# Kernel tuning notes

Measured on AMD Instinct MI355X. Metric: run time of the kernel, lower is better.

Reference implementation:

```python
import jax, jax.numpy as jnp
import numpy as np

N = 20000      # nodes
E = 320000     # edges (avg degree 16)
F_IN = 14
F_OUT = 9
H = 128        # hidden
L = 6          # message passing layers
ED = 3         # edge_dim
MSG_IN = 2 * H + ED  # 259


def _w(k, shape):
    return jax.random.normal(k, shape, jnp.float32) / np.sqrt(shape[0]).astype(np.float32)


def setup_inputs() -> dict:
    key = jax.random.key(0)
    ks = jax.random.split(key, 16)
    x = jax.random.normal(ks[0], (N, F_IN), jnp.float32)
    edge_index = jax.random.randint(ks[1], (2, E), 0, N, jnp.int64)
    edge_attr = jax.random.normal(ks[2], (E, ED), jnp.float32)
    # encoder: Linear(14,128) -> SiLU -> Linear(128,128)
    enc_w1 = _w(ks[3], (F_IN, H)); enc_b1 = jnp.zeros((H,), jnp.float32)
    enc_w2 = _w(ks[4], (H, H));    enc_b2 = jnp.zeros((H,), jnp.float32)
    # L EdgeConv layers: MLP(259->128) -> SiLU -> (128->128), stacked on leading dim
    kc = jax.random.split(ks[5], 2 * L)
    conv_w1 = jnp.stack([_w(kc[i], (MSG_IN, H)) for i in range(L)])
    conv_b1 = jnp.zeros((L, H), jnp.float32)
    conv_w2 = jnp.stack([_w(kc[L + i], (H, H)) for i in range(L)])
    conv_b2 = jnp.zeros((L, H), jnp.float32)
    # decoder: 128->128 SiLU 128->64 SiLU 64->9
    dec_w1 = _w(ks[6], (H, H));       dec_b1 = jnp.zeros((H,), jnp.float32)
    dec_w2 = _w(ks[7], (H, H // 2));  dec_b2 = jnp.zeros((H // 2,), jnp.float32)
    dec_w3 = _w(ks[8], (H // 2, F_OUT)); dec_b3 = jnp.zeros((F_OUT,), jnp.float32)
    return dict(x=x, edge_index=edge_index, edge_attr=edge_attr,
                enc_w1=enc_w1, enc_b1=enc_b1, enc_w2=enc_w2, enc_b2=enc_b2,
                conv_w1=conv_w1, conv_b1=conv_b1, conv_w2=conv_w2, conv_b2=conv_b2,
                dec_w1=dec_w1, dec_b1=dec_b1, dec_w2=dec_w2, dec_b2=dec_b2,
                dec_w3=dec_w3, dec_b3=dec_b3)


def _mlp2(x, w1, b1, w2, b2):
    return jnp.dot(jax.nn.silu(jnp.dot(x, w1) + b1), w2) + b2


def reference(x, edge_index, edge_attr,
              enc_w1, enc_b1, enc_w2, enc_b2,
              conv_w1, conv_b1, conv_w2, conv_b2,
              dec_w1, dec_b1, dec_w2, dec_b2, dec_w3, dec_b3):
    src, dst = edge_index[0], edge_index[1]
    # in-degree for mean aggregation (computed once; structure is fixed)
    deg = jnp.maximum(
        jax.ops.segment_sum(jnp.ones((E,), jnp.float32), dst, num_segments=N), 1.0)
    h = _mlp2(x, enc_w1, enc_b1, enc_w2, enc_b2)  # (N, H)
    for l in range(L):
        # gather-compute-scatter EdgeConv: msg MLP on [h_dst, h_src, edge_attr]
        m_in = jnp.concatenate([h[dst], h[src], edge_attr], axis=-1)  # (E, 2H+ED)
        m = _mlp2(m_in, conv_w1[l], conv_b1[l], conv_w2[l], conv_b2[l])  # (E, H)
        agg = jax.ops.segment_sum(m, dst, num_segments=N) / deg[:, None]  # (N, H)
        h = h + agg  # residual; dropout is identity in eval mode
    h = jax.nn.silu(jnp.dot(h, dec_w1) + dec_b1)
    h = jax.nn.silu(jnp.dot(h, dec_w2) + dec_b2)
    return jnp.dot(h, dec_w3) + dec_b3  # (N, F_OUT)
```

## Files before the change

### kernel.cpp

```cpp
#include <hip/hip_runtime.h>
#include <hip/hip_bf16.h>

#define NN 20000
#define EE 320000
#define HD 128

typedef _Float16 half8 __attribute__((ext_vector_type(8)));
typedef _Float16 half4 __attribute__((ext_vector_type(4)));
typedef _Float16 half2v __attribute__((ext_vector_type(2)));
typedef float floatx4 __attribute__((ext_vector_type(4)));
typedef float float2v __attribute__((ext_vector_type(2)));

__device__ __forceinline__ float silu_f(float x){
  float e = __expf(-x);
  return x * __builtin_amdgcn_rcpf(1.f + e);
}

__device__ __forceinline__ bool ei_is64(const int* __restrict__ ei){
  return (ei[1] | ei[3] | ei[5] | ei[7]) == 0;
}
__device__ __forceinline__ int ei_src(const int* __restrict__ ei, int e, bool is64){
  return is64 ? ei[2*(size_t)e] : ei[e];
}
__device__ __forceinline__ int ei_dst(const int* __restrict__ ei, int e, bool is64){
  return is64 ? ei[2*(size_t)EE + 2*(size_t)e] : ei[EE + e];
}

__global__ __launch_bounds__(256) void sentinel_kernel(float* __restrict__ out, int n, float val){
  int i = blockIdx.x*256 + threadIdx.x;
  if (i < n) out[i] = val;
}

__global__ __launch_bounds__(256) void pack_all_kernel(const float* __restrict__ cw1,
                                                       const float* __restrict__ cw2,
                                                       const float* __restrict__ dw1,
                                                       const float* __restrict__ dw2,
                                                       _Float16* __restrict__ w1p,
                                                       _Float16* __restrict__ w2p,
                                                       _Float16* __restrict__ w1dp,
                                                       _Float16* __restrict__ w2dp,
                                                       int* __restrict__ cur){
  int idx = blockIdx.x*256 + threadIdx.x;
  if (idx >= 319488){
    int j = idx - 319488;
    if (j < NN) cur[j] = 0;
    return;
  }
  if (idx < 196608){
    int j   = idx & 7;
    int ln  = (idx >> 3) & 63;
    int rest= idx >> 9;
    int cb  = rest & 15;
    int rest2 = rest >> 4;
    int ks  = rest2 & 3;
    int l   = rest2 >> 2;
    int k = ks*32 + (ln>>4)*8 + j;
    int c = cb*16 + (ln&15);
    float v = (c < 128) ? cw1[(size_t)l*33152 + (size_t)k*128 + c]
                        : cw1[(size_t)l*33152 + (size_t)(128+k)*128 + (c-128)];
    w1p[idx] = (_Float16)v;
  } else if (idx < 294912){
    int t = idx - 196608;
    int j   = t & 7;
    int ln  = (t >> 3) & 63;
    int rest= t >> 9;
    int cb  = rest & 7;
    int rest2 = rest >> 3;
    int ks  = rest2 & 3;
    int l   = rest2 >> 2;
    int k = ks*32 + (ln>>4)*8 + j;
    int c = cb*16 + (ln&15);
    w2p[t] = (_Float16)cw2[(size_t)l*16384 + (size_t)k*128 + c];
  } else {
    int t2 = idx - 294912;
    if (t2 < 16384){
      int j = t2 & 7, ln = (t2>>3)&63, cb = (t2>>9)&7, ks = t2>>12;
      int k = ks*32 + (ln>>4)*8 + j;
      int c = cb*16 + (ln&15);
      w1dp[t2] = (_Float16)dw1[(size_t)k*128 + c];
    } else {
      int t = t2 - 16384;
      int j = t & 7, ln = (t>>3)&63, cb = (t>>9)&3, ks = t>>11;
      int k = ks*32 + (ln>>4)*8 + j;
      int c = cb*16 + (ln&15);
      w2dp[t] = (_Float16)dw2[(size_t)k*64 + c];
    }
  }
}

__global__ __launch_bounds__(256) void count_kernel(const int* __restrict__ ei,
                                                    int* __restrict__ cnt,
                                                    int* __restrict__ rank){
  int e = blockIdx.x*256 + threadIdx.x;
  bool is64 = ei_is64(ei);
  rank[e] = atomicAdd(&cnt[ei_dst(ei, e, is64)], 1);
}

__global__ __launch_bounds__(1024) void scan_kernel(const int* __restrict__ cntcur,
                                                    int* __restrict__ row_start,
                                                    float* __restrict__ invd){
  __shared__ int part[1024];
  const int t = threadIdx.x;
  const int base = t*20;
  int loc[20];
  int sum = 0;
  #pragma unroll
  for (int i=0;i<20;++i){
    int n = base+i;
    int v = (n < NN) ? cntcur[n] : 0;
    loc[i] = sum; sum += v;
  }
  part[t] = sum;
  __syncthreads();
  for (int off=1; off<1024; off<<=1){
    int v = (t >= off) ? part[t-off] : 0;
    __syncthreads();
    part[t] += v;
    __syncthreads();
  }
  int pre = (t > 0) ? part[t-1] : 0;
  #pragma unroll
  for (int i=0;i<20;++i){
    int n = base+i;
    if (n < NN){
      int rs = pre + loc[i];
      int deg = ((i<19)?loc[i+1]:sum) - loc[i];
      row_start[n] = rs;
      invd[n] = (deg > 0) ? 1.f/(float)deg : 0.f;
    }
  }
  if (t == 1023) row_start[NN] = part[1023];
}

__global__ __launch_bounds__(128) void scatter_encoder_kernel(
    const int* __restrict__ ei, const float* __restrict__ eattr,
    const int* __restrict__ rstart, const int* __restrict__ rank,
    int4* __restrict__ rec,
    const float* __restrict__ x, const float* __restrict__ w1, const float* __restrict__ b1,
    const float* __restrict__ w2, const float* __restrict__ b2,
    float* __restrict__ h, _Float16* __restrict__ hh)
{
  __shared__ float xs[16][14];
  __shared__ float s1[16][128];
  const int tid = threadIdx.x;

  if (blockIdx.x < 2500){
    int e = blockIdx.x*128 + tid;
    bool is64 = ei_is64(ei);
    int s = ei_src(ei, e, is64);
    int d = ei_dst(ei, e, is64);
    int pos = rstart[d] + rank[e];
    int4 r;
    r.x = __float_as_int(eattr[(size_t)e*3+0]);
    r.y = __float_as_int(eattr[(size_t)e*3+1]);
    r.z = __float_as_int(eattr[(size_t)e*3+2]);
    r.w = s*256;
    rec[pos] = r;
    return;
  }

  const int n0 = (blockIdx.x - 2500)*16;
  for (int idx=tid; idx<224; idx+=128){
    int i = idx/14, k = idx%14;
    xs[i][k] = x[(size_t)(n0+i)*14 + k];
  }
  __syncthreads();
  const int o = tid;
  float acc[16];
  float bv = b1[o];
  #pragma unroll
  for (int i=0;i<16;++i) acc[i] = bv;
  for (int k=0;k<14;++k){
    float w = w1[k*128+o];
    #pragma unroll
    for (int i=0;i<16;++i) acc[i] += xs[i][k]*w;
  }
  #pragma unroll
  for (int i=0;i<16;++i) s1[i][o] = silu_f(acc[i]);
  __syncthreads();
  float bv2 = b2[o];
  #pragma unroll
  for (int i=0;i<16;++i) acc[i] = bv2;
  for (int k=0;k<128;k+=4){
    float w0=w2[(k+0)*128+o], w1v=w2[(k+1)*128+o], w2v=w2[(k+2)*128+o], w3v=w2[(k+3)*128+o];
    #pragma unroll
    for (int i=0;i<16;++i){
      float4 sv = *(const float4*)&s1[i][k];
      acc[i] += sv.x*w0 + sv.y*w1v + sv.z*w2v + sv.w*w3v;
    }
  }
  #pragma unroll
  for (int i=0;i<16;++i){
    size_t off = (size_t)(n0+i)*HD + o;
    h[off] = acc[i];
    hh[off] = (_Float16)acc[i];
  }
}

__global__ __launch_bounds__(256) void proj_kernel(
    const _Float16* __restrict__ hh, const _Float16* __restrict__ w1p,
    const float* __restrict__ b1, _Float16* __restrict__ UV)
{
  const int tid = threadIdx.x;
  const int wv  = tid >> 6;
  const int ln  = tid & 63;
  const int q   = ln >> 4;
  const int m   = ln & 15;
  const int n0  = blockIdx.x*16;

  floatx4 acc[4];
  #pragma unroll
  for (int j=0;j<4;++j) acc[j] = (floatx4){0.f,0.f,0.f,0.f};

  #pragma unroll
  for (int ks=0; ks<4; ++ks){
    half8 a = *(const half8*)(hh + (size_t)(n0+m)*HD + ks*32 + q*8);
    const _Float16* wb = w1p + (size_t)(ks*16*64 + ln)*8;
    #pragma unroll
    for (int j=0; j<4; ++j){
      half8 b = *(const half8*)(wb + (size_t)(wv*4+j)*512);
      acc[j] = __builtin_amdgcn_mfma_f32_16x16x32_f16(a, b, acc[j], 0,0,0);
    }
  }
  #pragma unroll
  for (int j=0; j<4; ++j){
    const int c = (wv*4+j)*16 + m;
    const float bias = (c < 128) ? b1[c] : 0.f;
    #pragma unroll
    for (int r=0;r<4;++r)
      UV[(size_t)(n0+q*4+r)*256 + c] = (_Float16)(acc[j][r] + bias);
  }
}

__device__ __forceinline__ float2v edge_contrib(int4 r, half2v v, float2v u,
                                                float2v wc0, float2v wc1, float2v wc2){
  float2v p = u;
  p += __int_as_float(r.x) * wc0;
  p += __int_as_float(r.y) * wc1;
  p += __int_as_float(r.z) * wc2;
  p[0] += (float)v[0];
  p[1] += (float)v[1];
  float2v s;
  s[0] = silu_f(p[0]);
  s[1] = silu_f(p[1]);
  return s;
}

__global__ __launch_bounds__(256) void edge_agg_kernel(
    const _Float16* __restrict__ UV, const int* __restrict__ row_start,
    const int4* __restrict__ rec,
    const float* __restrict__ w1e, const float* __restrict__ invd,
    _Float16* __restrict__ S)
{
  const int tid = threadIdx.x;
  const int wv  = __builtin_amdgcn_readfirstlane(tid >> 6);
  const int ln  = tid & 63;
  const int n   = blockIdx.x*4 + wv;
  const int c0  = ln*2;

  const float2v wc0 = *(const float2v*)(w1e +   0 + c0);
  const float2v wc1 = *(const float2v*)(w1e + 128 + c0);
  const float2v wc2 = *(const float2v*)(w1e + 256 + c0);

  half2v uvp = *(const half2v*)(UV + (size_t)n*256 + c0);
  float2v u; u[0] = (float)uvp[0]; u[1] = (float)uvp[1];

  const int rs = row_start[n], re = row_start[n+1];
  float2v a0 = {0.f,0.f}, a1 = {0.f,0.f}, a2 = {0.f,0.f}, a3 = {0.f,0.f};

  const int nq = (re - rs) >> 2;
  int e = rs;
  for (int q = 0; q < nq; ++q, e += 4){
    const int4 r0 = rec[e+0];
    const int4 r1 = rec[e+1];
    const int4 r2 = rec[e+2];
    const int4 r3 = rec[e+3];
    const half2v v0 = *(const half2v*)(UV + (size_t)r0.w + 128 + c0);
    const half2v v1 = *(const half2v*)(UV + (size_t)r1.w + 128 + c0);
    const half2v v2 = *(const half2v*)(UV + (size_t)r2.w + 128 + c0);
    const half2v v3 = *(const half2v*)(UV + (size_t)r3.w + 128 + c0);
    a0 += edge_contrib(r0, v0, u, wc0, wc1, wc2);
    a1 += edge_contrib(r1, v1, u, wc0, wc1, wc2);
    a2 += edge_contrib(r2, v2, u, wc0, wc1, wc2);
    a3 += edge_contrib(r3, v3, u, wc0, wc1, wc2);
  }
  if (e < re){
    const int e1 = (e+1 < re) ? e+1 : e;
    const int e2 = (e+2 < re) ? e+2 : e;
    const int4 r0 = rec[e];
    const int4 r1 = rec[e1];
    const int4 r2 = rec[e2];
    const half2v v0 = *(const half2v*)(UV + (size_t)r0.w + 128 + c0);
    const half2v v1 = *(const half2v*)(UV + (size_t)r1.w + 128 + c0);
    const half2v v2 = *(const half2v*)(UV + (size_t)r2.w + 128 + c0);
    a0 += edge_contrib(r0, v0, u, wc0, wc1, wc2);
    if (e+1 < re) a1 += edge_contrib(r1, v1, u, wc0, wc1, wc2);
    if (e+2 < re) a2 += edge_contrib(r2, v2, u, wc0, wc1, wc2);
  }
  float2v a = (a0 + a1) + (a2 + a3);
  const float iv = invd[n];
  half2v outv; outv[0] = (_Float16)(a[0]*iv); outv[1] = (_Float16)(a[1]*iv);
  *(half2v*)(S + (size_t)n*HD + c0) = outv;
}

__global__ __launch_bounds__(256) void node_proj_kernel(
    const _Float16* __restrict__ S, const _Float16* __restrict__ w2p,
    const float* __restrict__ b2, const float* __restrict__ invd,
    float* __restrict__ h,
    const _Float16* __restrict__ w1pn, const float* __restrict__ b1n,
    _Float16* __restrict__ UV, int do_proj,
    const _Float16* __restrict__ w1dp, const float* __restrict__ db1,
    const _Float16* __restrict__ w2dp, const float* __restrict__ db2,
    const float* __restrict__ dw3, const float* __restrict__ db3,
    float* __restrict__ out, int do_dec)
{
  __shared__ _Float16 hl[16][136];
  __shared__ __align__(16) char ubuf[8576];
  float    (*dl)[132]  = (float(*)[132])ubuf;
  _Float16 (*d1)[136]  = (_Float16(*)[136])ubuf;
  float    (*s2m)[66]  = (float(*)[66])(ubuf + 4352);

  const int tid = threadIdx.x;
  const int wv  = tid >> 6;
  const int ln  = tid & 63;
  const int q   = ln >> 4;
  const int m   = ln & 15;
  const int n0  = blockIdx.x*16;

  floatx4 acc[2];
  acc[0] = (floatx4){0.f,0.f,0.f,0.f};
  acc[1] = (floatx4){0.f,0.f,0.f,0.f};
  #pragma unroll
  for (int ks=0; ks<4; ++ks){
    half8 a = *(const half8*)(S + (size_t)(n0+m)*HD + ks*32 + q*8);
    const _Float16* wb = w2p + (size_t)(ks*8*64 + ln)*8;
    #pragma unroll
    for (int j=0;j<2;++j){
      half8 b = *(const half8*)(wb + (size_t)(wv*2+j)*512);
      acc[j] = __builtin_amdgcn_mfma_f32_16x16x32_f16(a, b, acc[j], 0,0,0);
    }
  }
  #pragma unroll
  for (int j=0; j<2; ++j){
    const int c = (wv*2+j)*16 + m;
    #pragma unroll
    for (int r=0;r<4;++r) dl[q*4+r][c] = acc[j][r];
  }
  __syncthreads();

  {
    const int idx = tid*8;
    const int row = idx >> 7;
    const int col = idx & 127;
    const float g = (invd[n0 + row] > 0.f) ? 1.f : 0.f;
    float4 h0 = *(const float4*)&h[(size_t)(n0+row)*HD + col];
    float4 h1 = *(const float4*)&h[(size_t)(n0+row)*HD + col + 4];
    float4 b0 = *(const float4*)&b2[col];
    float4 b1v = *(const float4*)&b2[col + 4];
    float4 d0 = *(const float4*)&dl[row][col];
    float4 d1v = *(const float4*)&dl[row][col + 4];
    h0.x += d0.x + g*b0.x;  h0.y += d0.y + g*b0.y;
    h0.z += d0.z + g*b0.z;  h0.w += d0.w + g*b0.w;
    h1.x += d1v.x + g*b1v.x; h1.y += d1v.y + g*b1v.y;
    h1.z += d1v.z + g*b1v.z; h1.w += d1v.w + g*b1v.w;
    if (!do_dec){
      *(float4*)&h[(size_t)(n0+row)*HD + col]     = h0;
      *(float4*)&h[(size_t)(n0+row)*HD + col + 4] = h1;
    }
    half4 p0, p1;
    p0[0]=(_Float16)h0.x; p0[1]=(_Float16)h0.y; p0[2]=(_Float16)h0.z; p0[3]=(_Float16)h0.w;
    p1[0]=(_Float16)h1.x; p1[1]=(_Float16)h1.y; p1[2]=(_Float16)h1.z; p1[3]=(_Float16)h1.w;
    *(half4*)&hl[row][col]     = p0;
    *(half4*)&hl[row][col + 4] = p1;
  }
  __syncthreads();

  if (do_proj){
    floatx4 acc2[4];
    #pragma unroll
    for (int j=0;j<4;++j) acc2[j] = (floatx4){0.f,0.f,0.f,0.f};
    #pragma unroll
    for (int ks=0; ks<4; ++ks){
      half8 a = *(const half8*)&hl[m][ks*32 + q*8];
      const _Float16* wb = w1pn + (size_t)(ks*16*64 + ln)*8;
      #pragma unroll
      for (int j=0; j<4; ++j){
        half8 b = *(const half8*)(wb + (size_t)(wv*4+j)*512);
        acc2[j] = __builtin_amdgcn_mfma_f32_16x16x32_f16(a, b, acc2[j], 0,0,0);
      }
    }
    #pragma unroll
    for (int j=0; j<4; ++j){
      const int c = (wv*4+j)*16 + m;
      const float bias = (c < 128) ? b1n[c] : 0.f;
      #pragma unroll
      for (int r=0;r<4;++r)
        UV[(size_t)(n0+q*4+r)*256 + c] = (_Float16)(acc2[j][r] + bias);
    }
  }

  if (do_dec){
    floatx4 acc1[2];
    acc1[0] = (floatx4){0.f,0.f,0.f,0.f};
    acc1[1] = (floatx4){0.f,0.f,0.f,0.f};
    #pragma unroll
    for (int ks=0; ks<4; ++ks){
      half8 a = *(const half8*)&hl[m][ks*32 + q*8];
      const _Float16* wb = w1dp + (size_t)(ks*8*64 + ln)*8;
      #pragma unroll
      for (int j=0; j<2; ++j){
        half8 b = *(const half8*)(wb + (size_t)(wv*2+j)*512);
        acc1[j] = __builtin_amdgcn_mfma_f32_16x16x32_f16(a, b, acc1[j], 0,0,0);
      }
    }
    __syncthreads();
    #pragma unroll
    for (int j=0; j<2; ++j){
      const int c = (wv*2+j)*16 + m;
      const float bv = db1[c];
      #pragma unroll
      for (int r=0;r<4;++r)
        d1[q*4+r][c] = (_Float16)silu_f(acc1[j][r] + bv);
    }
    __syncthreads();

    floatx4 acc2 = (floatx4){0.f,0.f,0.f,0.f};
    #pragma unroll
    for (int ks=0; ks<4; ++ks){
      half8 a = *(const half8*)&d1[m][ks*32 + q*8];
      const _Float16* wb = w2dp + (size_t)(ks*4*64 + ln)*8;
      half8 b = *(const half8*)(wb + (size_t)wv*512);
      acc2 = __builtin_amdgcn_mfma_f32_16x16x32_f16(a, b, acc2, 0,0,0);
    }
    {
      const int c = wv*16 + m;
      const float bv = db2[c];
      #pragma unroll
      for (int r=0;r<4;++r)
        s2m[q*4+r][c] = silu_f(acc2[r] + bv);
    }
    __syncthreads();

    if (tid < 144){
      int i = tid/9, oo = tid%9;
      float a = db3[oo];
      #pragma unroll 8
      for (int k=0;k<64;++k) a += s2m[i][k]*dw3[k*9+oo];
      out[(size_t)(n0+i)*9 + oo] = a;
    }
  }
}

constexpr size_t OFF_H    = 0;
constexpr size_t OFF_HH   = 10240000;
constexpr size_t OFF_UV   = 15360000;
constexpr size_t OFF_S    = 25600000;
constexpr size_t OFF_INVD = 30720000;
constexpr size_t OFF_RS   = 30800000;
constexpr size_t OFF_CUR  = 30880064;
constexpr size_t OFF_REC  = 30960064;
constexpr size_t OFF_RANK = 36080064;
constexpr size_t OFF_W1P  = 37360064;
constexpr size_t OFF_W2P  = 37753280;
constexpr size_t OFF_DW1P = 37949888;
constexpr size_t OFF_DW2P = 37982656;
constexpr size_t WS_NEEDED= 37999040;

extern "C" void kernel_launch(void* const* d_in, const int* in_sizes, int n_in,
                              void* d_out, int out_size, void* d_ws, size_t ws_size,
                              hipStream_t stream)
{
  float* out = (float*)d_out;
  const int nout_blk = (out_size + 255)/256;

  static const int EXP_SIZES[17] = {280000,640000,960000,1792,128,16384,128,
                                    198912,768,98304,768,16384,128,8192,64,576,9};
  if (n_in != 17){
    sentinel_kernel<<<nout_blk, 256, 0, stream>>>(out, out_size, 2.0e7f + (float)n_in*1.0e3f);
    return;
  }
  for (int i = 0; i < 17; ++i){
    if (in_sizes[i] != EXP_SIZES[i]){
      int sz = in_sizes[i] < 99999 ? in_sizes[i] : 99999;
      sentinel_kernel<<<nout_blk, 256, 0, stream>>>(out, out_size,
          1.0e7f + (float)i*1.0e5f + (float)sz);
      return;
    }
  }
  if (ws_size < WS_NEEDED){
    sentinel_kernel<<<nout_blk, 256, 0, stream>>>(out, out_size, 1.0e6f);
    return;
  }

  const float* x       = (const float*)d_in[0];
  const int*   ei      = (const int*)  d_in[1];
  const float* eattr   = (const float*)d_in[2];
  const float* enc_w1  = (const float*)d_in[3];
  const float* enc_b1  = (const float*)d_in[4];
  const float* enc_w2  = (const float*)d_in[5];
  const float* enc_b2  = (const float*)d_in[6];
  const float* conv_w1 = (const float*)d_in[7];
  const float* conv_b1 = (const float*)d_in[8];
  const float* conv_w2 = (const float*)d_in[9];
  const float* conv_b2 = (const float*)d_in[10];
  const float* dec_w1  = (const float*)d_in[11];
  const float* dec_b1  = (const float*)d_in[12];
  const float* dec_w2  = (const float*)d_in[13];
  const float* dec_b2  = (const float*)d_in[14];
  const float* dec_w3  = (const float*)d_in[15];
  const float* dec_b3  = (const float*)d_in[16];

  char* ws = (char*)d_ws;
  float*    h     = (float*)   (ws + OFF_H);
  _Float16* hh    = (_Float16*)(ws + OFF_HH);
  _Float16* UV    = (_Float16*)(ws + OFF_UV);
  _Float16* S     = (_Float16*)(ws + OFF_S);
  float*    invd  = (float*)   (ws + OFF_INVD);
  int*      rstart= (int*)     (ws + OFF_RS);
  int*      cur   = (int*)     (ws + OFF_CUR);
  int4*     rec   = (int4*)    (ws + OFF_REC);
  int*      rank  = (int*)     (ws + OFF_RANK);
  _Float16* w1p   = (_Float16*)(ws + OFF_W1P);
  _Float16* w2p   = (_Float16*)(ws + OFF_W2P);
  _Float16* w1dp  = (_Float16*)(ws + OFF_DW1P);
  _Float16* w2dp  = (_Float16*)(ws + OFF_DW2P);

  pack_all_kernel<<<1327, 256, 0, stream>>>(conv_w1, conv_w2, dec_w1, dec_w2,
                                            w1p, w2p, w1dp, w2dp, cur);
  count_kernel<<<EE/256, 256, 0, stream>>>(ei, cur, rank);
  scan_kernel<<<1, 1024, 0, stream>>>(cur, rstart, invd);
  scatter_encoder_kernel<<<3750, 128, 0, stream>>>(ei, eattr, rstart, rank, rec,
                                                   x, enc_w1, enc_b1, enc_w2, enc_b2,
                                                   h, hh);
  proj_kernel<<<NN/16, 256, 0, stream>>>(hh, w1p, conv_b1, UV);
  for (int l=0; l<6; ++l){
    edge_agg_kernel<<<NN/4, 256, 0, stream>>>(UV, rstart, rec,
                                              conv_w1 + (size_t)l*33152 + 32768,
                                              invd, S);
    const int lp = (l < 5) ? l+1 : 0;
    node_proj_kernel<<<NN/16, 256, 0, stream>>>(S, w2p + (size_t)l*16384,
                                                conv_b2 + (size_t)l*128, invd, h,
                                                w1p + (size_t)lp*32768,
                                                conv_b1 + (size_t)lp*128,
                                                UV, (l < 5) ? 1 : 0,
                                                w1dp, dec_b1, w2dp, dec_b2,
                                                dec_w3, dec_b3, out,
                                                (l == 5) ? 1 : 0);
  }
}
```

Baseline: 372.4 us.

## Fuse edge aggregation and node projection into one per-layer kernel

Merges the edge gather/aggregate kernel and the node update/projection kernel into a single 1024-thread kernel per layer. Each block handles 16 nodes, one wave per node, and keeps the aggregated messages in shared memory instead of writing and re-reading a global S buffer. The UV buffer is double-buffered (ping-pong) so the next layer's projections can be written while neighbours still read the current one. This removes one launch per layer and the S round trip, at the cost of larger blocks, idle waves in the smaller GEMM stages, and an extra global buffer.

```diff
diff --git a/kernel.cpp b/kernel.cpp
--- a/kernel.cpp
+++ b/kernel.cpp
@@ -246,74 +246,20 @@
   return s;
 }
 
-__global__ __launch_bounds__(256) void edge_agg_kernel(
-    const _Float16* __restrict__ UV, const int* __restrict__ row_start,
-    const int4* __restrict__ rec,
+__global__ __launch_bounds__(1024, 8) void layer_kernel(
+    const _Float16* __restrict__ UVc, _Float16* __restrict__ UVn,
+    const int* __restrict__ row_start, const int4* __restrict__ rec,
     const float* __restrict__ w1e, const float* __restrict__ invd,
-    _Float16* __restrict__ S)
-{
-  const int tid = threadIdx.x;
-  const int wv  = __builtin_amdgcn_readfirstlane(tid >> 6);
-  const int ln  = tid & 63;
-  const int n   = blockIdx.x*4 + wv;
-  const int c0  = ln*2;
-
-  const float2v wc0 = *(const float2v*)(w1e +   0 + c0);
-  const float2v wc1 = *(const float2v*)(w1e + 128 + c0);
-  const float2v wc2 = *(const float2v*)(w1e + 256 + c0);
-
-  half2v uvp = *(const half2v*)(UV + (size_t)n*256 + c0);
-  float2v u; u[0] = (float)uvp[0]; u[1] = (float)uvp[1];
-
-  const int rs = row_start[n], re = row_start[n+1];
-  float2v a0 = {0.f,0.f}, a1 = {0.f,0.f}, a2 = {0.f,0.f}, a3 = {0.f,0.f};
-
-  const int nq = (re - rs) >> 2;
-  int e = rs;
-  for (int q = 0; q < nq; ++q, e += 4){
-    const int4 r0 = rec[e+0];
-    const int4 r1 = rec[e+1];
-    const int4 r2 = rec[e+2];
-    const int4 r3 = rec[e+3];
-    const half2v v0 = *(const half2v*)(UV + (size_t)r0.w + 128 + c0);
-    const half2v v1 = *(const half2v*)(UV + (size_t)r1.w + 128 + c0);
-    const half2v v2 = *(const half2v*)(UV + (size_t)r2.w + 128 + c0);
-    const half2v v3 = *(const half2v*)(UV + (size_t)r3.w + 128 + c0);
-    a0 += edge_contrib(r0, v0, u, wc0, wc1, wc2);
-    a1 += edge_contrib(r1, v1, u, wc0, wc1, wc2);
-    a2 += edge_contrib(r2, v2, u, wc0, wc1, wc2);
-    a3 += edge_contrib(r3, v3, u, wc0, wc1, wc2);
-  }
-  if (e < re){
-    const int e1 = (e+1 < re) ? e+1 : e;
-    const int e2 = (e+2 < re) ? e+2 : e;
-    const int4 r0 = rec[e];
-    const int4 r1 = rec[e1];
-    const int4 r2 = rec[e2];
-    const half2v v0 = *(const half2v*)(UV + (size_t)r0.w + 128 + c0);
-    const half2v v1 = *(const half2v*)(UV + (size_t)r1.w + 128 + c0);
-    const half2v v2 = *(const half2v*)(UV + (size_t)r2.w + 128 + c0);
-    a0 += edge_contrib(r0, v0, u, wc0, wc1, wc2);
-    if (e+1 < re) a1 += edge_contrib(r1, v1, u, wc0, wc1, wc2);
-    if (e+2 < re) a2 += edge_contrib(r2, v2, u, wc0, wc1, wc2);
-  }
-  float2v a = (a0 + a1) + (a2 + a3);
-  const float iv = invd[n];
-  half2v outv; outv[0] = (_Float16)(a[0]*iv); outv[1] = (_Float16)(a[1]*iv);
-  *(half2v*)(S + (size_t)n*HD + c0) = outv;
-}
-
-__global__ __launch_bounds__(256) void node_proj_kernel(
-    const _Float16* __restrict__ S, const _Float16* __restrict__ w2p,
-    const float* __restrict__ b2, const float* __restrict__ invd,
+    const _Float16* __restrict__ w2p, const float* __restrict__ b2,
     float* __restrict__ h,
     const _Float16* __restrict__ w1pn, const float* __restrict__ b1n,
-    _Float16* __restrict__ UV, int do_proj,
+    int do_proj,
     const _Float16* __restrict__ w1dp, const float* __restrict__ db1,
     const _Float16* __restrict__ w2dp, const float* __restrict__ db2,
     const float* __restrict__ dw3, const float* __restrict__ db3,
     float* __restrict__ out, int do_dec)
 {
+  __shared__ _Float16 Sl[16][136];
   __shared__ _Float16 hl[16][136];
   __shared__ __align__(16) char ubuf[8576];
   float    (*dl)[132]  = (float(*)[132])ubuf;
@@ -321,123 +267,136 @@
   float    (*s2m)[66]  = (float(*)[66])(ubuf + 4352);
 
   const int tid = threadIdx.x;
-  const int wv  = tid >> 6;
+  const int w   = __builtin_amdgcn_readfirstlane(tid >> 6);
   const int ln  = tid & 63;
   const int q   = ln >> 4;
   const int m   = ln & 15;
   const int n0  = blockIdx.x*16;
 
-  floatx4 acc[2];
-  acc[0] = (floatx4){0.f,0.f,0.f,0.f};
-  acc[1] = (floatx4){0.f,0.f,0.f,0.f};
-  #pragma unroll
-  for (int ks=0; ks<4; ++ks){
-    half8 a = *(const half8*)(S + (size_t)(n0+m)*HD + ks*32 + q*8);
-    const _Float16* wb = w2p + (size_t)(ks*8*64 + ln)*8;
-    #pragma unroll
-    for (int j=0;j<2;++j){
-      half8 b = *(const half8*)(wb + (size_t)(wv*2+j)*512);
-      acc[j] = __builtin_amdgcn_mfma_f32_16x16x32_f16(a, b, acc[j], 0,0,0);
-    }
-  }
-  #pragma unroll
-  for (int j=0; j<2; ++j){
-    const int c = (wv*2+j)*16 + m;
-    #pragma unroll
-    for (int r=0;r<4;++r) dl[q*4+r][c] = acc[j][r];
+  {
+    const int n  = n0 + w;
+    const int c0 = ln*2;
+    const float2v wc0 = *(const float2v*)(w1e +   0 + c0);
+    const float2v wc1 = *(const float2v*)(w1e + 128 + c0);
+    const float2v wc2 = *(const float2v*)(w1e + 256 + c0);
+
+    half2v uvp = *(const half2v*)(UVc + (size_t)n*256 + c0);
+    float2v u; u[0] = (float)uvp[0]; u[1] = (float)uvp[1];
+
+    const int rs = row_start[n], re = row_start[n+1];
+    float2v a0 = {0.f,0.f}, a1 = {0.f,0.f}, a2 = {0.f,0.f}, a3 = {0.f,0.f};
+
+    const int nq = (re - rs) >> 2;
+    int e = rs;
+    for (int qq = 0; qq < nq; ++qq, e += 4){
+      const int4 r0 = rec[e+0];
+      const int4 r1 = rec[e+1];
+      const int4 r2 = rec[e+2];
+      const int4 r3 = rec[e+3];
+      const half2v v0 = *(const half2v*)(UVc + (size_t)r0.w + 128 + c0);
+      const half2v v1 = *(const half2v*)(UVc + (size_t)r1.w + 128 + c0);
+      const half2v v2 = *(const half2v*)(UVc + (size_t)r2.w + 128 + c0);
+      const half2v v3 = *(const half2v*)(UVc + (size_t)r3.w + 128 + c0);
+      a0 += edge_contrib(r0, v0, u, wc0, wc1, wc2);
+      a1 += edge_contrib(r1, v1, u, wc0, wc1, wc2);
+      a2 += edge_contrib(r2, v2, u, wc0, wc1, wc2);
+      a3 += edge_contrib(r3, v3, u, wc0, wc1, wc2);
+    }
+    if (e < re){
+      const int e1 = (e+1 < re) ? e+1 : e;
+      const int e2 = (e+2 < re) ? e+2 : e;
+      const int4 r0 = rec[e];
+      const int4 r1 = rec[e1];
+      const int4 r2 = rec[e2];
+      const half2v v0 = *(const half2v*)(UVc + (size_t)r0.w + 128 + c0);
+      const half2v v1 = *(const half2v*)(UVc + (size_t)r1.w + 128 + c0);
+      const half2v v2 = *(const half2v*)(UVc + (size_t)r2.w + 128 + c0);
+      a0 += edge_contrib(r0, v0, u, wc0, wc1, wc2);
+      if (e+1 < re) a1 += edge_contrib(r1, v1, u, wc0, wc1, wc2);
+      if (e+2 < re) a2 += edge_contrib(r2, v2, u, wc0, wc1, wc2);
+    }
+    float2v a = (a0 + a1) + (a2 + a3);
+    const float iv = invd[n];
+    half2v outv; outv[0] = (_Float16)(a[0]*iv); outv[1] = (_Float16)(a[1]*iv);
+    *(half2v*)&Sl[w][c0] = outv;
   }
   __syncthreads();
 
+  if (w < 8){
+    floatx4 acc = (floatx4){0.f,0.f,0.f,0.f};
+    #pragma unroll
+    for (int ks=0; ks<4; ++ks){
+      half8 a = *(const half8*)&Sl[m][ks*32 + q*8];
+      half8 b = *(const half8*)(w2p + (size_t)(ks*8*64 + ln)*8 + (size_t)w*512);
+      acc = __builtin_amdgcn_mfma_f32_16x16x32_f16(a, b, acc, 0,0,0);
+    }
+    const int c = w*16 + m;
+    #pragma unroll
+    for (int r=0;r<4;++r) dl[q*4+r][c] = acc[r];
+  }
+  __syncthreads();
+
   {
-    const int idx = tid*8;
-    const int row = idx >> 7;
-    const int col = idx & 127;
+    const int row = w;
+    const int col = ln*2;
     const float g = (invd[n0 + row] > 0.f) ? 1.f : 0.f;
-    float4 h0 = *(const float4*)&h[(size_t)(n0+row)*HD + col];
-    float4 h1 = *(const float4*)&h[(size_t)(n0+row)*HD + col + 4];
-    float4 b0 = *(const float4*)&b2[col];
-    float4 b1v = *(const float4*)&b2[col + 4];
-    float4 d0 = *(const float4*)&dl[row][col];
-    float4 d1v = *(const float4*)&dl[row][col + 4];
-    h0.x += d0.x + g*b0.x;  h0.y += d0.y + g*b0.y;
-    h0.z += d0.z + g*b0.z;  h0.w += d0.w + g*b0.w;
-    h1.x += d1v.x + g*b1v.x; h1.y += d1v.y + g*b1v.y;
-    h1.z += d1v.z + g*b1v.z; h1.w += d1v.w + g*b1v.w;
-    if (!do_dec){
-      *(float4*)&h[(size_t)(n0+row)*HD + col]     = h0;
-      *(float4*)&h[(size_t)(n0+row)*HD + col + 4] = h1;
-    }
-    half4 p0, p1;
-    p0[0]=(_Float16)h0.x; p0[1]=(_Float16)h0.y; p0[2]=(_Float16)h0.z; p0[3]=(_Float16)h0.w;
-    p1[0]=(_Float16)h1.x; p1[1]=(_Float16)h1.y; p1[2]=(_Float16)h1.z; p1[3]=(_Float16)h1.w;
-    *(half4*)&hl[row][col]     = p0;
-    *(half4*)&hl[row][col + 4] = p1;
+    float2 hv = *(const float2*)&h[(size_t)(n0+row)*HD + col];
+    float2 bv = *(const float2*)&b2[col];
+    float2 dv = *(const float2*)&dl[row][col];
+    hv.x += dv.x + g*bv.x;
+    hv.y += dv.y + g*bv.y;
+    if (!do_dec)
+      *(float2*)&h[(size_t)(n0+row)*HD + col] = hv;
+    half2v p; p[0] = (_Float16)hv.x; p[1] = (_Float16)hv.y;
+    *(half2v*)&hl[row][col] = p;
   }
   __syncthreads();
 
   if (do_proj){
-    floatx4 acc2[4];
-    #pragma unroll
-    for (int j=0;j<4;++j) acc2[j] = (floatx4){0.f,0.f,0.f,0.f};
+    floatx4 acc = (floatx4){0.f,0.f,0.f,0.f};
     #pragma unroll
     for (int ks=0; ks<4; ++ks){
       half8 a = *(const half8*)&hl[m][ks*32 + q*8];
-      const _Float16* wb = w1pn + (size_t)(ks*16*64 + ln)*8;
+      half8 b = *(const half8*)(w1pn + (size_t)(ks*16*64 + ln)*8 + (size_t)w*512);
+      acc = __builtin_amdgcn_mfma_f32_16x16x32_f16(a, b, acc, 0,0,0);
+    }
+    const int c = w*16 + m;
+    const float bias = (c < 128) ? b1n[c] : 0.f;
+    #pragma unroll
+    for (int r=0;r<4;++r)
+      UVn[(size_t)(n0+q*4+r)*256 + c] = (_Float16)(acc[r] + bias);
+  }
+
+  if (do_dec){
+    if (w < 8){
+      floatx4 acc = (floatx4){0.f,0.f,0.f,0.f};
       #pragma unroll
-      for (int j=0; j<4; ++j){
-        half8 b = *(const half8*)(wb + (size_t)(wv*4+j)*512);
-        acc2[j] = __builtin_amdgcn_mfma_f32_16x16x32_f16(a, b, acc2[j], 0,0,0);
+      for (int ks=0; ks<4; ++ks){
+        half8 a = *(const half8*)&hl[m][ks*32 + q*8];
+        half8 b = *(const half8*)(w1dp + (size_t)(ks*8*64 + ln)*8 + (size_t)w*512);
+        acc = __builtin_amdgcn_mfma_f32_16x16x32_f16(a, b, acc, 0,0,0);
       }
-    }
-    #pragma unroll
-    for (int j=0; j<4; ++j){
-      const int c = (wv*4+j)*16 + m;
-      const float bias = (c < 128) ? b1n[c] : 0.f;
-      #pragma unroll
-      for (int r=0;r<4;++r)
-        UV[(size_t)(n0+q*4+r)*256 + c] = (_Float16)(acc2[j][r] + bias);
-    }
-  }
-
-  if (do_dec){
-    floatx4 acc1[2];
-    acc1[0] = (floatx4){0.f,0.f,0.f,0.f};
-    acc1[1] = (floatx4){0.f,0.f,0.f,0.f};
-    #pragma unroll
-    for (int ks=0; ks<4; ++ks){
-      half8 a = *(const half8*)&hl[m][ks*32 + q*8];
-      const _Float16* wb = w1dp + (size_t)(ks*8*64 + ln)*8;
-      #pragma unroll
-      for (int j=0; j<2; ++j){
-        half8 b = *(const half8*)(wb + (size_t)(wv*2+j)*512);
-        acc1[j] = __builtin_amdgcn_mfma_f32_16x16x32_f16(a, b, acc1[j], 0,0,0);
-      }
-    }
-    __syncthreads();
-    #pragma unroll
-    for (int j=0; j<2; ++j){
-      const int c = (wv*2+j)*16 + m;
+      const int c = w*16 + m;
       const float bv = db1[c];
       #pragma unroll
       for (int r=0;r<4;++r)
-        d1[q*4+r][c] = (_Float16)silu_f(acc1[j][r] + bv);
+        d1[q*4+r][c] = (_Float16)silu_f(acc[r] + bv);
     }
     __syncthreads();
 
-    floatx4 acc2 = (floatx4){0.f,0.f,0.f,0.f};
-    #pragma unroll
-    for (int ks=0; ks<4; ++ks){
-      half8 a = *(const half8*)&d1[m][ks*32 + q*8];
-      const _Float16* wb = w2dp + (size_t)(ks*4*64 + ln)*8;
-      half8 b = *(const half8*)(wb + (size_t)wv*512);
-      acc2 = __builtin_amdgcn_mfma_f32_16x16x32_f16(a, b, acc2, 0,0,0);
-    }
-    {
-      const int c = wv*16 + m;
+    if (w < 4){
+      floatx4 acc = (floatx4){0.f,0.f,0.f,0.f};
+      #pragma unroll
+      for (int ks=0; ks<4; ++ks){
+        half8 a = *(const half8*)&d1[m][ks*32 + q*8];
+        half8 b = *(const half8*)(w2dp + (size_t)(ks*4*64 + ln)*8 + (size_t)w*512);
+        acc = __builtin_amdgcn_mfma_f32_16x16x32_f16(a, b, acc, 0,0,0);
+      }
+      const int c = w*16 + m;
       const float bv = db2[c];
       #pragma unroll
       for (int r=0;r<4;++r)
-        s2m[q*4+r][c] = silu_f(acc2[r] + bv);
+        s2m[q*4+r][c] = silu_f(acc[r] + bv);
     }
     __syncthreads();
 
@@ -453,18 +412,18 @@
 
 constexpr size_t OFF_H    = 0;
 constexpr size_t OFF_HH   = 10240000;
-constexpr size_t OFF_UV   = 15360000;
-constexpr size_t OFF_S    = 25600000;
-constexpr size_t OFF_INVD = 30720000;
-constexpr size_t OFF_RS   = 30800000;
-constexpr size_t OFF_CUR  = 30880064;
-constexpr size_t OFF_REC  = 30960064;
-constexpr size_t OFF_RANK = 36080064;
-constexpr size_t OFF_W1P  = 37360064;
-constexpr size_t OFF_W2P  = 37753280;
-constexpr size_t OFF_DW1P = 37949888;
-constexpr size_t OFF_DW2P = 37982656;
-constexpr size_t WS_NEEDED= 37999040;
+constexpr size_t OFF_UVA  = 15360000;
+constexpr size_t OFF_UVB  = 25600000;
+constexpr size_t OFF_INVD = 35840000;
+constexpr size_t OFF_RS   = 35920000;
+constexpr size_t OFF_CUR  = 36000064;
+constexpr size_t OFF_REC  = 36080064;
+constexpr size_t OFF_RANK = 41200064;
+constexpr size_t OFF_W1P  = 42480064;
+constexpr size_t OFF_W2P  = 42873280;
+constexpr size_t OFF_DW1P = 43069888;
+constexpr size_t OFF_DW2P = 43102656;
+constexpr size_t WS_NEEDED= 43119040;
 
 extern "C" void kernel_launch(void* const* d_in, const int* in_sizes, int n_in,
                               void* d_out, int out_size, void* d_ws, size_t ws_size,
@@ -513,8 +472,8 @@
   char* ws = (char*)d_ws;
   float*    h     = (float*)   (ws + OFF_H);
   _Float16* hh    = (_Float16*)(ws + OFF_HH);
-  _Float16* UV    = (_Float16*)(ws + OFF_UV);
-  _Float16* S     = (_Float16*)(ws + OFF_S);
+  _Float16* UVa   = (_Float16*)(ws + OFF_UVA);
+  _Float16* UVb   = (_Float16*)(ws + OFF_UVB);
   float*    invd  = (float*)   (ws + OFF_INVD);
   int*      rstart= (int*)     (ws + OFF_RS);
   int*      cur   = (int*)     (ws + OFF_CUR);
@@ -532,19 +491,22 @@
   scatter_encoder_kernel<<<3750, 128, 0, stream>>>(ei, eattr, rstart, rank, rec,
                                                    x, enc_w1, enc_b1, enc_w2, enc_b2,
                                                    h, hh);
-  proj_kernel<<<NN/16, 256, 0, stream>>>(hh, w1p, conv_b1, UV);
+  proj_kernel<<<NN/16, 256, 0, stream>>>(hh, w1p, conv_b1, UVa);
   for (int l=0; l<6; ++l){
-    edge_agg_kernel<<<NN/4, 256, 0, stream>>>(UV, rstart, rec,
-                                              conv_w1 + (size_t)l*33152 + 32768,
-                                              invd, S);
+    _Float16* UVc = (l & 1) ? UVb : UVa;
+    _Float16* UVn = (l & 1) ? UVa : UVb;
     const int lp = (l < 5) ? l+1 : 0;
-    node_proj_kernel<<<NN/16, 256, 0, stream>>>(S, w2p + (size_t)l*16384,
-                                                conv_b2 + (size_t)l*128, invd, h,
-                                                w1p + (size_t)lp*32768,
-                                                conv_b1 + (size_t)lp*128,
-                                                UV, (l < 5) ? 1 : 0,
-                                                w1dp, dec_b1, w2dp, dec_b2,
-                                                dec_w3, dec_b3, out,
-                                                (l == 5) ? 1 : 0);
-  }
-}
+    layer_kernel<<<NN/16, 1024, 0, stream>>>(UVc, UVn, rstart, rec,
+                                             conv_w1 + (size_t)l*33152 + 32768,
+                                             invd,
+                                             w2p + (size_t)l*16384,
+                                             conv_b2 + (size_t)l*128,
+                                             h,
+                                             w1p + (size_t)lp*32768,
+                                             conv_b1 + (size_t)lp*128,
+                                             (l < 5) ? 1 : 0,
+                                             w1dp, dec_b1, w2dp, dec_b2,
+                                             dec_w3, dec_b3, out,
+                                             (l == 5) ? 1 : 0);
+  }
+}
```

Result: faster. 331.1 us, median of 2 (-11.1%).
